# Kernel tuning notes

Hardware: AMD Instinct MI355X
Metric: run time of the kernel (lower is better)

## Reference

```python
import jax, jax.numpy as jnp
import numpy as np

N_USERS = 100000
N_ITEMS = 50000
N = N_USERS + N_ITEMS  # graph nodes
E = 2_400_000
B = 16384
EMB = 64
HID = 128
LN_EPS = 1e-5


def _gcn(x, W, b, src, dst):
    # PyG GCNConv (eval): sym-normalized aggregation with self-loops.
    xw = x @ W                                      # [N, out]
    deg = jnp.ones((N,), x.dtype).at[dst].add(1.0)  # in-degree + self-loop
    dinv = jax.lax.rsqrt(deg)
    norm = dinv[src] * dinv[dst]                    # [E]
    msg = xw[src] * norm[:, None]                   # [E, out] gather
    out = jax.ops.segment_sum(msg, dst, num_segments=N)
    out = out + xw * (dinv * dinv)[:, None]         # self-loop term (norm_ii = 1/deg_i)
    return out + b


def _ln(h, g, b):
    mu = jnp.mean(h, axis=-1, keepdims=True)
    var = jnp.mean(jnp.square(h - mu), axis=-1, keepdims=True)
    return (h - mu) * jax.lax.rsqrt(var + LN_EPS) * g + b


def setup_inputs() -> dict:
    key = jax.random.key(0)
    ks = jax.random.split(key, 20)
    f32 = jnp.float32
    def lin(k, fi, fo):
        return jax.random.normal(k, (fi, fo), f32) * (1.0 / np.sqrt(fi))
    inp = {
        "x": jax.random.normal(ks[0], (N, EMB), f32),
        "src": jax.random.randint(ks[1], (E,), 0, N, jnp.int32),
        "dst": jax.random.randint(ks[2], (E,), 0, N, jnp.int32),
        "user_indices": jax.random.randint(ks[3], (B,), 1, N_USERS + 1, jnp.int32),
        "item_indices": jax.random.randint(ks[4], (B,), 1, N_ITEMS + 1, jnp.int32),
        # GCNConv weights
        "W1": lin(ks[5], EMB, HID), "b1": jnp.zeros((HID,), f32),
        "W2": lin(ks[6], HID, EMB), "b2": jnp.zeros((EMB,), f32),
        # MLP head: Linear(128,128)-LN-ReLU-Linear(128,64)-LN-ReLU-Linear(64,1)
        "fcW1": lin(ks[7], 2 * EMB, HID), "fcb1": jnp.zeros((HID,), f32),
        "g1": jnp.ones((HID,), f32), "be1": jnp.zeros((HID,), f32),
        "fcW2": lin(ks[8], HID, HID // 2), "fcb2": jnp.zeros((HID // 2,), f32),
        "g2": jnp.ones((HID // 2,), f32), "be2": jnp.zeros((HID // 2,), f32),
        "fcW3": lin(ks[9], HID // 2, 1), "fcb3": jnp.zeros((1,), f32),
    }
    return inp


def reference(x, src, dst, user_indices, item_indices,
              W1, b1, W2, b2,
              fcW1, fcb1, g1, be1, fcW2, fcb2, g2, be2, fcW3, fcb3):
    # graph path (edge_index and x provided); dropout inactive in eval mode
    h = jax.nn.relu(_gcn(x, W1, b1, src, dst))
    h = _gcn(h, W2, b2, src, dst)                   # [N, EMB]
    user_emb = h[:N_USERS][user_indices - 1]        # [B, EMB]
    item_emb = h[N_USERS:][item_indices - 1]        # [B, EMB]
    c = jnp.concatenate([user_emb, item_emb], axis=1)  # [B, 2*EMB]
    z = jax.nn.relu(_ln(c @ fcW1 + fcb1, g1, be1))
    z = jax.nn.relu(_ln(z @ fcW2 + fcb2, g2, be2))
    z = z @ fcW3 + fcb3                             # [B, 1]
    return jax.nn.sigmoid(z).squeeze()
```

## Files before the change

kernel.cpp:

```cpp
#include <hip/hip_runtime.h>
#include <hip/hip_bf16.h>
#include <math.h>

#define N_USERS_C 100000
#define BK_SHIFT 9
#define BK_NODES 512
#define CPAD 16

typedef __bf16 bf8_t __attribute__((ext_vector_type(8)));
typedef float f32x4 __attribute__((ext_vector_type(4)));

__device__ __forceinline__ unsigned int pack_bf16(float a, float b) {
    __hip_bfloat16 ha = __float2bfloat16(a), hb = __float2bfloat16(b);
    return ((unsigned int)(*(unsigned short*)&hb) << 16) | (unsigned int)(*(unsigned short*)&ha);
}
__device__ __forceinline__ unsigned short bf16_1(float a) {
    __hip_bfloat16 ha = __float2bfloat16(a);
    return *(unsigned short*)&ha;
}
__device__ __forceinline__ float bf_lo(unsigned int u) { return __uint_as_float(u << 16); }
__device__ __forceinline__ float bf_hi(unsigned int u) { return __uint_as_float(u & 0xffff0000u); }

__global__ __launch_bounds__(512) void k_pre(const int* __restrict__ dst, int* __restrict__ chist,
                                             const float* __restrict__ x, unsigned int* __restrict__ xb,
                                             const float* __restrict__ W1, const float* __restrict__ W2,
                                             unsigned int* __restrict__ w1p, unsigned int* __restrict__ w2p,
                                             int E, int nbk, int EB2, int n2, int XB) {
    __shared__ int lcnt[BK_NODES];
    const int bid = blockIdx.x;
    const int t = threadIdx.x;
    if (bid < EB2) {
        if (t < nbk) lcnt[t] = 0;
        __syncthreads();
        int e0 = bid * 4096;
        #pragma unroll
        for (int j = 0; j < 8; ++j) {
            int e = e0 + j * 512 + t;
            if (e < E) atomicAdd(&lcnt[dst[e] >> BK_SHIFT], 1);
        }
        __syncthreads();
        if (t < nbk && lcnt[t]) atomicAdd(&chist[t * CPAD], lcnt[t]);
    } else if (bid < EB2 + XB) {
        int base = (bid - EB2) * 2048;
        #pragma unroll
        for (int j = 0; j < 4; ++j) {
            int i = base + j * 512 + t;
            if (i < n2) {
                float2 v = ((const float2*)x)[i];
                xb[i] = pack_bf16(v.x, v.y);
            }
        }
    } else if (bid == EB2 + XB) {
        #pragma unroll
        for (int j = 0; j < 8; ++j) {
            int i = j * 512 + t;
            int kp = i >> 7, n = i & 127;
            w1p[n * 32 + kp] = pack_bf16(W1[(size_t)(2 * kp) * 128 + n],
                                         W1[(size_t)(2 * kp + 1) * 128 + n]);
        }
    } else {
        #pragma unroll
        for (int j = 0; j < 8; ++j) {
            int i = j * 512 + t;
            int kp = i >> 6, n = i & 63;
            w2p[n * 64 + kp] = pack_bf16(W2[(size_t)(2 * kp) * 64 + n],
                                         W2[(size_t)(2 * kp + 1) * 64 + n]);
        }
    }
}

__global__ __launch_bounds__(512) void k_bin(const int* __restrict__ src,
                                             const int* __restrict__ dst,
                                             const int* __restrict__ chist,
                                             int* __restrict__ bcursor0,
                                             int* __restrict__ pairBuf, int E, int nbk) {
    __shared__ int lcnt[BK_NODES];
    __shared__ int lofs[BK_NODES];
    __shared__ int delta[BK_NODES];
    __shared__ int waveSum[8];
    __shared__ int sPack[4096];
    __shared__ unsigned short sBkt[4096];
    const int t = threadIdx.x;
    const int lane = t & 63;
    const int w = t >> 6;
    const int e0 = blockIdx.x * 4096;
    if (t < nbk) lcnt[t] = 0;
    __syncthreads();

    int mySrc[8], myB[8], myDl[8];
    #pragma unroll
    for (int j = 0; j < 8; ++j) {
        int e = e0 + j * 512 + t;
        if (e < E) {
            int sv = src[e], dv = dst[e];
            mySrc[j] = sv; myB[j] = dv >> BK_SHIFT; myDl[j] = dv & (BK_NODES - 1);
            atomicAdd(&lcnt[myB[j]], 1);
        } else myB[j] = -1;
    }
    __syncthreads();

    int v = (t < nbk) ? lcnt[t] : 0;
    int inc = v;
    #pragma unroll
    for (int off = 1; off < 64; off <<= 1) {
        int n = __shfl_up(inc, off);
        if (lane >= off) inc += n;
    }
    if (lane == 63) waveSum[w] = inc;
    int cv = (t < nbk) ? chist[t * CPAD] : 0;
    int cinc = cv;
    #pragma unroll
    for (int off = 1; off < 64; off <<= 1) {
        int n = __shfl_up(cinc, off);
        if (lane >= off) cinc += n;
    }
    __shared__ int cWaveSum[8];
    if (lane == 63) cWaveSum[w] = cinc;
    __syncthreads();
    int wp = 0, cwp = 0;
    #pragma unroll
    for (int i = 0; i < 8; ++i) {
        wp += (i < w) ? waveSum[i] : 0;
        cwp += (i < w) ? cWaveSum[i] : 0;
    }
    int ex = wp + inc - v;
    int cbase = cwp + cinc - cv;
    if (t < nbk) {
        lofs[t] = ex;
        int gb = cbase + ((v > 0) ? atomicAdd(&bcursor0[t * CPAD], v) : 0);
        delta[t] = gb - ex;
    }
    __syncthreads();

    #pragma unroll
    for (int j = 0; j < 8; ++j) {
        if (myB[j] >= 0) {
            int p = atomicAdd(&lofs[myB[j]], 1);
            sPack[p] = mySrc[j] | (myDl[j] << 18);
            sBkt[p] = (unsigned short)myB[j];
        }
    }
    __syncthreads();
    int total = (E - e0 < 4096) ? (E - e0) : 4096;
    for (int i = t; i < total; i += 512)
        pairBuf[delta[sBkt[i]] + i] = sPack[i];
}

__global__ __launch_bounds__(512) void k_bscatter(const int* __restrict__ pairBuf,
                                                  const int* __restrict__ chist,
                                                  int* __restrict__ rowstart,
                                                  float* __restrict__ dinv,
                                                  int* __restrict__ csr, int N, int E, int nbk) {
    const int b = blockIdx.x;
    const int n0 = b << BK_SHIFT;
    int nn = N - n0; if (nn > BK_NODES) nn = BK_NODES;
    __shared__ int hist[BK_NODES];
    __shared__ int curs[BK_NODES];
    __shared__ int waveSum[8];
    __shared__ int sE0, sE1;
    const int t = threadIdx.x;
    const int lane = t & 63;
    const int w = t >> 6;

    {
        int cv = (t < nbk) ? chist[t * CPAD] : 0;
        int cinc = cv;
        #pragma unroll
        for (int off = 1; off < 64; off <<= 1) {
            int n = __shfl_up(cinc, off);
            if (lane >= off) cinc += n;
        }
        if (lane == 63) waveSum[w] = cinc;
        if (t < nn) hist[t] = 0;
        __syncthreads();
        int cwp = 0;
        #pragma unroll
        for (int i = 0; i < 8; ++i) cwp += (i < w) ? waveSum[i] : 0;
        if (t == b) { sE0 = cwp + cinc - cv; sE1 = cwp + cinc; }
    }
    __syncthreads();
    const int e0 = sE0, e1 = sE1;

    for (int e = e0 + t; e < e1; e += 512)
        atomicAdd(&hist[pairBuf[e] >> 18], 1);
    __syncthreads();

    int v = (t < nn) ? hist[t] : 0;
    int inc = v;
    #pragma unroll
    for (int off = 1; off < 64; off <<= 1) {
        int n = __shfl_up(inc, off);
        if (lane >= off) inc += n;
    }
    if (lane == 63) waveSum[w] = inc;
    __syncthreads();
    int wp = 0;
    #pragma unroll
    for (int i = 0; i < 8; ++i) wp += (i < w) ? waveSum[i] : 0;
    int ex = wp + inc - v;
    if (t < nn) {
        int r = e0 + ex;
        rowstart[n0 + t] = r;
        curs[t] = r;
        dinv[n0 + t] = rsqrtf((float)(v + 1));
    }
    if (b == gridDim.x - 1 && t == 0) rowstart[N] = E;
    __syncthreads();
    for (int e = e0 + t; e < e1; e += 512) {
        int pk = pairBuf[e];
        int pos = atomicAdd(&curs[pk >> 18], 1);
        csr[pos] = pk & 0x3FFFF;
    }
}

__global__ __launch_bounds__(256) void k_gather1(const int* __restrict__ rowstart,
                                                 const int* __restrict__ csr,
                                                 const float* __restrict__ dinv,
                                                 const uint4* __restrict__ xb4,
                                                 unsigned int* __restrict__ outb, int N) {
    const int node = blockIdx.x * 4 + (threadIdx.x >> 6);
    const int l = threadIdx.x & 63;
    if (node >= N) return;
    const int sub = l >> 3;
    const int c = l & 7;
    const int rs = rowstart[node];
    const int re = rowstart[node + 1];

    float acc[8] = {0.f, 0.f, 0.f, 0.f, 0.f, 0.f, 0.f, 0.f};
    for (int base = rs; base < re; base += 64) {
        int idx = base + l;
        int sE = (idx < re) ? csr[idx] : 0;
        float dE = (idx < re) ? dinv[sE] : 0.0f;
        int cnt = re - base; if (cnt > 64) cnt = 64;
        int groups = (cnt + 7) >> 3;
        for (int g = 0; g < groups; ++g) {
            int e = g * 8 + sub;
            int sk = __shfl(sE, e);
            float dk = __shfl(dE, e);
            uint4 u = xb4[(size_t)sk * 8 + c];
            acc[0] += dk * bf_lo(u.x); acc[1] += dk * bf_hi(u.x);
            acc[2] += dk * bf_lo(u.y); acc[3] += dk * bf_hi(u.y);
            acc[4] += dk * bf_lo(u.z); acc[5] += dk * bf_hi(u.z);
            acc[6] += dk * bf_lo(u.w); acc[7] += dk * bf_hi(u.w);
        }
    }
    #pragma unroll
    for (int m = 8; m < 64; m <<= 1)
        #pragma unroll
        for (int i = 0; i < 8; ++i) acc[i] += __shfl_xor(acc[i], m);
    if (sub == 0) {
        float dd = dinv[node];
        float d2 = dd * dd;
        uint4 us = xb4[(size_t)node * 8 + c];
        uint4 o;
        o.x = pack_bf16(dd * acc[0] + d2 * bf_lo(us.x), dd * acc[1] + d2 * bf_hi(us.x));
        o.y = pack_bf16(dd * acc[2] + d2 * bf_lo(us.y), dd * acc[3] + d2 * bf_hi(us.y));
        o.z = pack_bf16(dd * acc[4] + d2 * bf_lo(us.z), dd * acc[5] + d2 * bf_hi(us.z));
        o.w = pack_bf16(dd * acc[6] + d2 * bf_lo(us.w), dd * acc[7] + d2 * bf_hi(us.w));
        ((uint4*)outb)[(size_t)node * 8 + c] = o;
    }
}

__global__ __launch_bounds__(256) void k_layer12(const unsigned int* __restrict__ aggXb,
                                                 const unsigned int* __restrict__ w1p,
                                                 const float* __restrict__ b1,
                                                 const unsigned int* __restrict__ w2p,
                                                 const float* __restrict__ dinv,
                                                 unsigned int* __restrict__ xs2b, int N) {
    __shared__ unsigned int sA[64 * 36];
    __shared__ unsigned int sB[128 * 36];
    __shared__ unsigned int sC[64 * 68];
    const int t = threadIdx.x;
    const int w = t >> 6;
    const int l = t & 63;
    const int n16 = l & 15;
    const int quad = l >> 4;
    const int row0 = blockIdx.x * 64;

    for (int i = t; i < 512; i += 256) {
        int r = i >> 3, c = i & 7;
        int row = row0 + r;
        uint4 u = (row < N) ? ((const uint4*)aggXb)[(size_t)row * 8 + c]
                            : make_uint4(0u, 0u, 0u, 0u);
        *(uint4*)&sA[r * 36 + c * 4] = u;
    }
    {
        const uint4* w1p4 = (const uint4*)w1p;
        for (int j = t; j < 1024; j += 256) {
            int n = j >> 3, kp4 = j & 7;
            *(uint4*)&sB[n * 36 + kp4 * 4] = w1p4[j];
        }
    }
    __syncthreads();

    f32x4 acc[8];
    #pragma unroll
    for (int nt = 0; nt < 8; ++nt) acc[nt] = (f32x4){0.f, 0.f, 0.f, 0.f};
    {
        const int am = w * 16 + n16;
        bf8_t a0 = *(const bf8_t*)&sA[am * 36 + quad * 4];
        bf8_t a1 = *(const bf8_t*)&sA[am * 36 + 16 + quad * 4];
        #pragma unroll
        for (int nt = 0; nt < 8; ++nt) {
            bf8_t b0 = *(const bf8_t*)&sB[(nt * 16 + n16) * 36 + quad * 4];
            bf8_t b1v = *(const bf8_t*)&sB[(nt * 16 + n16) * 36 + 16 + quad * 4];
            acc[nt] = __builtin_amdgcn_mfma_f32_16x16x32_bf16(a0, b0, acc[nt], 0, 0, 0);
            acc[nt] = __builtin_amdgcn_mfma_f32_16x16x32_bf16(a1, b1v, acc[nt], 0, 0, 0);
        }
    }
    __syncthreads();

    {
        unsigned short* sC16 = (unsigned short*)sC;
        #pragma unroll
        for (int nt = 0; nt < 8; ++nt) {
            int col = nt * 16 + n16;
            float bv = b1[col];
            #pragma unroll
            for (int reg = 0; reg < 4; ++reg) {
                int r = w * 16 + quad * 4 + reg;
                sC16[r * 136 + col] = bf16_1(fmaxf(acc[nt][reg] + bv, 0.f));
            }
        }
    }
    {
        const uint4* w2p4 = (const uint4*)w2p;
        for (int j = t; j < 1024; j += 256) {
            int n = j >> 4, kp4 = j & 15;
            *(uint4*)&sB[n * 68 + kp4 * 4] = w2p4[j];
        }
    }
    __syncthreads();

    f32x4 acc2[4];
    #pragma unroll
    for (int nt = 0; nt < 4; ++nt) acc2[nt] = (f32x4){0.f, 0.f, 0.f, 0.f};
    {
        const int am = w * 16 + n16;
        #pragma unroll
        for (int ks = 0; ks < 4; ++ks) {
            bf8_t a = *(const bf8_t*)&sC[am * 68 + ks * 16 + quad * 4];
            #pragma unroll
            for (int nt = 0; nt < 4; ++nt) {
                bf8_t b = *(const bf8_t*)&sB[(nt * 16 + n16) * 68 + ks * 16 + quad * 4];
                acc2[nt] = __builtin_amdgcn_mfma_f32_16x16x32_bf16(a, b, acc2[nt], 0, 0, 0);
            }
        }
    }

    __syncthreads();
    {
        unsigned short* sA16 = (unsigned short*)sA;
        #pragma unroll
        for (int reg = 0; reg < 4; ++reg) {
            int r = w * 16 + quad * 4 + reg;
            int row = row0 + r;
            float dd = (row < N) ? dinv[row] : 0.f;
            #pragma unroll
            for (int nt = 0; nt < 4; ++nt)
                sA16[r * 72 + nt * 16 + n16] = bf16_1(acc2[nt][reg] * dd);
        }
    }
    __syncthreads();
    for (int i = t; i < 512; i += 256) {
        int r = i >> 3, c = i & 7;
        int row = row0 + r;
        if (row < N)
            ((uint4*)xs2b)[(size_t)row * 8 + c] = *(uint4*)&sA[r * 36 + c * 4];
    }
}

__global__ __launch_bounds__(256) void k_gather_pairs(const int* __restrict__ rowstart,
                                                      const int* __restrict__ csr,
                                                      const float* __restrict__ dinv,
                                                      const uint4* __restrict__ xs2b4,
                                                      const float* __restrict__ b2,
                                                      const int* __restrict__ ui,
                                                      const int* __restrict__ ii,
                                                      float* __restrict__ cB, int B) {
    const int wave = threadIdx.x >> 6;
    const int b = blockIdx.x * 2 + (wave >> 1);
    const int half = wave & 1;
    const int l = threadIdx.x & 63;
    const int sub = l >> 3;
    const int c = l & 7;
    if (b >= B) return;
    const int node = (half == 0) ? (ui[b] - 1) : (N_USERS_C + ii[b] - 1);
    const int rs = rowstart[node];
    const int re = rowstart[node + 1];

    float acc[8] = {0.f, 0.f, 0.f, 0.f, 0.f, 0.f, 0.f, 0.f};
    for (int base = rs; base < re; base += 64) {
        int idx = base + l;
        int sE = (idx < re) ? csr[idx] : 0;
        float vE = (idx < re) ? 1.0f : 0.0f;
        int cnt = re - base; if (cnt > 64) cnt = 64;
        int groups = (cnt + 7) >> 3;
        for (int g = 0; g < groups; ++g) {
            int e = g * 8 + sub;
            int sk = __shfl(sE, e);
            float vk = __shfl(vE, e);
            uint4 u = xs2b4[(size_t)sk * 8 + c];
            acc[0] += vk * bf_lo(u.x); acc[1] += vk * bf_hi(u.x);
            acc[2] += vk * bf_lo(u.y); acc[3] += vk * bf_hi(u.y);
            acc[4] += vk * bf_lo(u.z); acc[5] += vk * bf_hi(u.z);
            acc[6] += vk * bf_lo(u.w); acc[7] += vk * bf_hi(u.w);
        }
    }
    #pragma unroll
    for (int m = 8; m < 64; m <<= 1)
        #pragma unroll
        for (int i = 0; i < 8; ++i) acc[i] += __shfl_xor(acc[i], m);
    if (sub == 0) {
        float dd = dinv[node];
        uint4 us = xs2b4[(size_t)node * 8 + c];
        float4 s0, s1;
        s0.x = bf_lo(us.x); s0.y = bf_hi(us.x); s0.z = bf_lo(us.y); s0.w = bf_hi(us.y);
        s1.x = bf_lo(us.z); s1.y = bf_hi(us.z); s1.z = bf_lo(us.w); s1.w = bf_hi(us.w);
        float4 bb0 = ((const float4*)b2)[c * 2];
        float4 bb1 = ((const float4*)b2)[c * 2 + 1];
        float4 o0, o1;
        o0.x = dd * (acc[0] + s0.x) + bb0.x;
        o0.y = dd * (acc[1] + s0.y) + bb0.y;
        o0.z = dd * (acc[2] + s0.z) + bb0.z;
        o0.w = dd * (acc[3] + s0.w) + bb0.w;
        o1.x = dd * (acc[4] + s1.x) + bb1.x;
        o1.y = dd * (acc[5] + s1.y) + bb1.y;
        o1.z = dd * (acc[6] + s1.z) + bb1.z;
        o1.w = dd * (acc[7] + s1.w) + bb1.w;
        ((float4*)cB)[(size_t)b * 32 + half * 16 + c * 2] = o0;
        ((float4*)cB)[(size_t)b * 32 + half * 16 + c * 2 + 1] = o1;
    }
}

__global__ __launch_bounds__(256) void k_mlp(const float* __restrict__ cB,
                                             const float* __restrict__ fcW1, const float* __restrict__ fcb1,
                                             const float* __restrict__ g1,   const float* __restrict__ be1,
                                             const float* __restrict__ fcW2, const float* __restrict__ fcb2,
                                             const float* __restrict__ g2,   const float* __restrict__ be2,
                                             const float* __restrict__ fcW3, const float* __restrict__ fcb3,
                                             float* __restrict__ out) {
    __shared__ float sIn[32 * 128];
    __shared__ float sW[64 * 128];
    const int t = threadIdx.x;
    const int row0 = blockIdx.x * 32;
    const int rg = t >> 4;
    const int cg = t & 15;

    for (int i = t; i < 1024; i += 256) {
        int r = i >> 5, c4 = i & 31;
        *(float4*)&sIn[r * 128 + c4 * 4] = *(const float4*)&cB[(size_t)(row0 + r) * 128 + c4 * 4];
    }

    float acc1[2][8];
    {
        float4 b01 = *(const float4*)&fcb1[cg * 8];
        float4 b23 = *(const float4*)&fcb1[cg * 8 + 4];
        #pragma unroll
        for (int jj = 0; jj < 2; ++jj) {
            acc1[jj][0] = b01.x; acc1[jj][1] = b01.y; acc1[jj][2] = b01.z; acc1[jj][3] = b01.w;
            acc1[jj][4] = b23.x; acc1[jj][5] = b23.y; acc1[jj][6] = b23.z; acc1[jj][7] = b23.w;
        }
    }
    for (int s = 0; s < 2; ++s) {
        __syncthreads();
        for (int i = t; i < 2048; i += 256) {
            int k = i >> 5, c4 = i & 31;
            *(float4*)&sW[k * 128 + c4 * 4] = *(const float4*)&fcW1[(size_t)(64 * s + k) * 128 + c4 * 4];
        }
        __syncthreads();
        for (int k0 = 0; k0 < 64; k0 += 4) {
            float4 a[2];
            #pragma unroll
            for (int jj = 0; jj < 2; ++jj)
                a[jj] = *(const float4*)&sIn[(rg * 2 + jj) * 128 + 64 * s + k0];
            #pragma unroll
            for (int kk = 0; kk < 4; ++kk) {
                float4 w0 = *(const float4*)&sW[(k0 + kk) * 128 + cg * 8];
                float4 w1 = *(const float4*)&sW[(k0 + kk) * 128 + cg * 8 + 4];
                #pragma unroll
                for (int jj = 0; jj < 2; ++jj) {
                    float f = ((const float*)&a[jj])[kk];
                    acc1[jj][0] += f * w0.x; acc1[jj][1] += f * w0.y;
                    acc1[jj][2] += f * w0.z; acc1[jj][3] += f * w0.w;
                    acc1[jj][4] += f * w1.x; acc1[jj][5] += f * w1.y;
                    acc1[jj][6] += f * w1.z; acc1[jj][7] += f * w1.w;
                }
            }
        }
    }
    __syncthreads();

    {
        float4 g01 = *(const float4*)&g1[cg * 8];
        float4 g23 = *(const float4*)&g1[cg * 8 + 4];
        float4 e01 = *(const float4*)&be1[cg * 8];
        float4 e23 = *(const float4*)&be1[cg * 8 + 4];
        float gv[8] = {g01.x, g01.y, g01.z, g01.w, g23.x, g23.y, g23.z, g23.w};
        float ev[8] = {e01.x, e01.y, e01.z, e01.w, e23.x, e23.y, e23.z, e23.w};
        #pragma unroll
        for (int jj = 0; jj < 2; ++jj) {
            float s_ = 0.f, ss = 0.f;
            #pragma unroll
            for (int c = 0; c < 8; ++c) { float v = acc1[jj][c]; s_ += v; ss += v * v; }
            #pragma unroll
            for (int m = 1; m < 16; m <<= 1) { s_ += __shfl_xor(s_, m); ss += __shfl_xor(ss, m); }
            float mu = s_ * (1.0f / 128.0f);
            float var = ss * (1.0f / 128.0f) - mu * mu;
            float rs = rsqrtf(var + 1e-5f);
            #pragma unroll
            for (int c = 0; c < 8; ++c) {
                float z = (acc1[jj][c] - mu) * rs * gv[c] + ev[c];
                sIn[(rg * 2 + jj) * 128 + cg * 8 + c] = fmaxf(z, 0.f);
            }
        }
    }
    __syncthreads();

    for (int i = t; i < 2048; i += 256) {
        int k = i >> 4, c4 = i & 15;
        *(float4*)&sW[k * 64 + c4 * 4] = *(const float4*)&fcW2[(size_t)k * 64 + c4 * 4];
    }
    float acc2[2][4];
    {
        float4 bv = *(const float4*)&fcb2[cg * 4];
        #pragma unroll
        for (int jj = 0; jj < 2; ++jj) {
            acc2[jj][0] = bv.x; acc2[jj][1] = bv.y; acc2[jj][2] = bv.z; acc2[jj][3] = bv.w;
        }
    }
    __syncthreads();
    for (int k0 = 0; k0 < 128; k0 += 4) {
        float4 a[2], w[4];
        #pragma unroll
        for (int jj = 0; jj < 2; ++jj) a[jj] = *(const float4*)&sIn[(rg * 2 + jj) * 128 + k0];
        #pragma unroll
        for (int kk = 0; kk < 4; ++kk) w[kk] = *(const float4*)&sW[(k0 + kk) * 64 + cg * 4];
        #pragma unroll
        for (int jj = 0; jj < 2; ++jj) {
            const float* aj = (const float*)&a[jj];
            #pragma unroll
            for (int kk = 0; kk < 4; ++kk) {
                float f = aj[kk];
                acc2[jj][0] += f * w[kk].x; acc2[jj][1] += f * w[kk].y;
                acc2[jj][2] += f * w[kk].z; acc2[jj][3] += f * w[kk].w;
            }
        }
    }

    {
        float4 gv4 = *(const float4*)&g2[cg * 4];
        float4 ev4 = *(const float4*)&be2[cg * 4];
        float4 w34 = *(const float4*)&fcW3[cg * 4];
        float gv[4] = {gv4.x, gv4.y, gv4.z, gv4.w};
        float ev[4] = {ev4.x, ev4.y, ev4.z, ev4.w};
        float wv[4] = {w34.x, w34.y, w34.z, w34.w};
        float b3 = fcb3[0];
        #pragma unroll
        for (int jj = 0; jj < 2; ++jj) {
            float s_ = 0.f, ss = 0.f;
            #pragma unroll
            for (int c = 0; c < 4; ++c) { float v = acc2[jj][c]; s_ += v; ss += v * v; }
            #pragma unroll
            for (int m = 1; m < 16; m <<= 1) { s_ += __shfl_xor(s_, m); ss += __shfl_xor(ss, m); }
            float mu = s_ * (1.0f / 64.0f);
            float var = ss * (1.0f / 64.0f) - mu * mu;
            float rs = rsqrtf(var + 1e-5f);
            float p = 0.f;
            #pragma unroll
            for (int c = 0; c < 4; ++c) {
                float z = fmaxf((acc2[jj][c] - mu) * rs * gv[c] + ev[c], 0.f);
                p += z * wv[c];
            }
            #pragma unroll
            for (int m = 1; m < 16; m <<= 1) p += __shfl_xor(p, m);
            if (cg == 0) out[row0 + rg * 2 + jj] = 1.0f / (1.0f + expf(-(p + b3)));
        }
    }
}

extern "C" void kernel_launch(void* const* d_in, const int* in_sizes, int n_in,
                              void* d_out, int out_size, void* d_ws, size_t ws_size,
                              hipStream_t stream) {
    const float* x    = (const float*)d_in[0];
    const int*   src  = (const int*)d_in[1];
    const int*   dst  = (const int*)d_in[2];
    const int*   ui   = (const int*)d_in[3];
    const int*   ii   = (const int*)d_in[4];
    const float* W1   = (const float*)d_in[5];
    const float* b1   = (const float*)d_in[6];
    const float* W2   = (const float*)d_in[7];
    const float* b2   = (const float*)d_in[8];
    const float* fcW1 = (const float*)d_in[9];
    const float* fcb1 = (const float*)d_in[10];
    const float* g1   = (const float*)d_in[11];
    const float* be1  = (const float*)d_in[12];
    const float* fcW2 = (const float*)d_in[13];
    const float* fcb2 = (const float*)d_in[14];
    const float* g2   = (const float*)d_in[15];
    const float* be2  = (const float*)d_in[16];
    const float* fcW3 = (const float*)d_in[17];
    const float* fcb3 = (const float*)d_in[18];
    float* out = (float*)d_out;

    const int N = in_sizes[0] / 64;
    const int E = in_sizes[1];
    const int B = in_sizes[3];
    const int NBK = (N + BK_NODES - 1) >> BK_SHIFT;
    const int EB2 = (E + 4095) / 4096;
    const int n2 = N * 32;
    const int XB = (n2 + 2047) / 2048;

    float* ws   = (float*)d_ws;
    float* dinv = ws;
    int* rowstart = (int*)(dinv + N);
    int* csr      = rowstart + (N + 1);
    unsigned int* xb = (unsigned int*)(csr + E);
    unsigned int* bufU = xb + (size_t)N * 32;
    unsigned int* xs2b = bufU + (size_t)N * 32;
    float* cB = (float*)(xs2b + (size_t)N * 32);
    unsigned int* w1p = (unsigned int*)(cB + (size_t)B * 128);
    unsigned int* w2p = w1p + 4096;
    int* pairBuf = (int*)bufU;
    int* chist   = pairBuf + E;
    int* bcursor = chist + 512 * CPAD;
    unsigned int* aggXb = bufU;

    hipMemsetAsync(chist, 0, 2 * 512 * CPAD * sizeof(int), stream);
    k_pre<<<EB2 + XB + 2, 512, 0, stream>>>(dst, chist, x, xb, W1, W2, w1p, w2p,
                                            E, NBK, EB2, n2, XB);
    k_bin<<<EB2, 512, 0, stream>>>(src, dst, chist, bcursor, pairBuf, E, NBK);
    k_bscatter<<<NBK, 512, 0, stream>>>(pairBuf, chist, rowstart, dinv, csr, N, E, NBK);

    k_gather1<<<(N + 3) / 4, 256, 0, stream>>>(rowstart, csr, dinv, (const uint4*)xb, aggXb, N);

    k_layer12<<<(N + 63) / 64, 256, 0, stream>>>(aggXb, w1p, b1, w2p, dinv, xs2b, N);

    k_gather_pairs<<<(B + 1) / 2, 256, 0, stream>>>(rowstart, csr, dinv, (const uint4*)xs2b,
                                                    b2, ui, ii, cB, B);

    k_mlp<<<B / 32, 256, 0, stream>>>(cB, fcW1, fcb1, g1, be1,
                                      fcW2, fcb2, g2, be2, fcW3, fcb3, out);
}
```

Before: 336.2 us.

## Prescale node features by dinv in bscatter and software-pipeline gather loads

The bf16 node features are pre-multiplied by their own deg^-1/2 inside k_bscatter, so k_gather1 no longer does a per-edge dinv gather or multiply, and the self-loop term becomes dd*(acc+self). Both gather kernels now prefetch the next edge group's feature row before accumulating the current one, and they load the self row and dinv early to overlap latency. The cost is an extra read-modify-write pass over xb in bscatter and an additional bf16 rounding of the scaled features.

```diff
diff --git a/kernel.cpp b/kernel.cpp
--- a/kernel.cpp
+++ b/kernel.cpp
@@ -150,12 +150,15 @@
                                                   const int* __restrict__ chist,
                                                   int* __restrict__ rowstart,
                                                   float* __restrict__ dinv,
-                                                  int* __restrict__ csr, int N, int E, int nbk) {
+                                                  int* __restrict__ csr,
+                                                  unsigned int* __restrict__ xb,
+                                                  int N, int E, int nbk) {
     const int b = blockIdx.x;
     const int n0 = b << BK_SHIFT;
     int nn = N - n0; if (nn > BK_NODES) nn = BK_NODES;
     __shared__ int hist[BK_NODES];
     __shared__ int curs[BK_NODES];
+    __shared__ float sdv[BK_NODES];
     __shared__ int waveSum[8];
     __shared__ int sE0, sE1;
     const int t = threadIdx.x;
@@ -202,7 +205,9 @@
         int r = e0 + ex;
         rowstart[n0 + t] = r;
         curs[t] = r;
-        dinv[n0 + t] = rsqrtf((float)(v + 1));
+        float dv = rsqrtf((float)(v + 1));
+        dinv[n0 + t] = dv;
+        sdv[t] = dv;
     }
     if (b == gridDim.x - 1 && t == 0) rowstart[N] = E;
     __syncthreads();
@@ -210,6 +215,19 @@
         int pk = pairBuf[e];
         int pos = atomicAdd(&curs[pk >> 18], 1);
         csr[pos] = pk & 0x3FFFF;
+    }
+    {
+        uint4* xb4 = (uint4*)(xb + (size_t)n0 * 32);
+        int tot = nn * 8;
+        for (int j = t; j < tot; j += 512) {
+            float dv = sdv[j >> 3];
+            uint4 u = xb4[j];
+            u.x = pack_bf16(dv * bf_lo(u.x), dv * bf_hi(u.x));
+            u.y = pack_bf16(dv * bf_lo(u.y), dv * bf_hi(u.y));
+            u.z = pack_bf16(dv * bf_lo(u.z), dv * bf_hi(u.z));
+            u.w = pack_bf16(dv * bf_lo(u.w), dv * bf_hi(u.w));
+            xb4[j] = u;
+        }
     }
 }
 
@@ -225,23 +243,29 @@
     const int c = l & 7;
     const int rs = rowstart[node];
     const int re = rowstart[node + 1];
+    uint4 us = xb4[(size_t)node * 8 + c];
+    float dd = dinv[node];
 
     float acc[8] = {0.f, 0.f, 0.f, 0.f, 0.f, 0.f, 0.f, 0.f};
     for (int base = rs; base < re; base += 64) {
         int idx = base + l;
         int sE = (idx < re) ? csr[idx] : 0;
-        float dE = (idx < re) ? dinv[sE] : 0.0f;
         int cnt = re - base; if (cnt > 64) cnt = 64;
         int groups = (cnt + 7) >> 3;
+        int sk = __shfl(sE, sub);
+        uint4 u = xb4[(size_t)sk * 8 + c];
         for (int g = 0; g < groups; ++g) {
-            int e = g * 8 + sub;
-            int sk = __shfl(sE, e);
-            float dk = __shfl(dE, e);
-            uint4 u = xb4[(size_t)sk * 8 + c];
-            acc[0] += dk * bf_lo(u.x); acc[1] += dk * bf_hi(u.x);
-            acc[2] += dk * bf_lo(u.y); acc[3] += dk * bf_hi(u.y);
-            acc[4] += dk * bf_lo(u.z); acc[5] += dk * bf_hi(u.z);
-            acc[6] += dk * bf_lo(u.w); acc[7] += dk * bf_hi(u.w);
+            uint4 ucur = u;
+            if (g + 1 < groups) {
+                int skn = __shfl(sE, (g + 1) * 8 + sub);
+                u = xb4[(size_t)skn * 8 + c];
+            }
+            if (g * 8 + sub < cnt) {
+                acc[0] += bf_lo(ucur.x); acc[1] += bf_hi(ucur.x);
+                acc[2] += bf_lo(ucur.y); acc[3] += bf_hi(ucur.y);
+                acc[4] += bf_lo(ucur.z); acc[5] += bf_hi(ucur.z);
+                acc[6] += bf_lo(ucur.w); acc[7] += bf_hi(ucur.w);
+            }
         }
     }
     #pragma unroll
@@ -249,14 +273,11 @@
         #pragma unroll
         for (int i = 0; i < 8; ++i) acc[i] += __shfl_xor(acc[i], m);
     if (sub == 0) {
-        float dd = dinv[node];
-        float d2 = dd * dd;
-        uint4 us = xb4[(size_t)node * 8 + c];
         uint4 o;
-        o.x = pack_bf16(dd * acc[0] + d2 * bf_lo(us.x), dd * acc[1] + d2 * bf_hi(us.x));
-        o.y = pack_bf16(dd * acc[2] + d2 * bf_lo(us.y), dd * acc[3] + d2 * bf_hi(us.y));
-        o.z = pack_bf16(dd * acc[4] + d2 * bf_lo(us.z), dd * acc[5] + d2 * bf_hi(us.z));
-        o.w = pack_bf16(dd * acc[6] + d2 * bf_lo(us.w), dd * acc[7] + d2 * bf_hi(us.w));
+        o.x = pack_bf16(dd * (acc[0] + bf_lo(us.x)), dd * (acc[1] + bf_hi(us.x)));
+        o.y = pack_bf16(dd * (acc[2] + bf_lo(us.y)), dd * (acc[3] + bf_hi(us.y)));
+        o.z = pack_bf16(dd * (acc[4] + bf_lo(us.z)), dd * (acc[5] + bf_hi(us.z)));
+        o.w = pack_bf16(dd * (acc[6] + bf_lo(us.w)), dd * (acc[7] + bf_hi(us.w)));
         ((uint4*)outb)[(size_t)node * 8 + c] = o;
     }
 }
@@ -388,23 +409,29 @@
     const int node = (half == 0) ? (ui[b] - 1) : (N_USERS_C + ii[b] - 1);
     const int rs = rowstart[node];
     const int re = rowstart[node + 1];
+    uint4 us = xs2b4[(size_t)node * 8 + c];
+    float dd = dinv[node];
 
     float acc[8] = {0.f, 0.f, 0.f, 0.f, 0.f, 0.f, 0.f, 0.f};
     for (int base = rs; base < re; base += 64) {
         int idx = base + l;
         int sE = (idx < re) ? csr[idx] : 0;
-        float vE = (idx < re) ? 1.0f : 0.0f;
         int cnt = re - base; if (cnt > 64) cnt = 64;
         int groups = (cnt + 7) >> 3;
+        int sk = __shfl(sE, sub);
+        uint4 u = xs2b4[(size_t)sk * 8 + c];
         for (int g = 0; g < groups; ++g) {
-            int e = g * 8 + sub;
-            int sk = __shfl(sE, e);
-            float vk = __shfl(vE, e);
-            uint4 u = xs2b4[(size_t)sk * 8 + c];
-            acc[0] += vk * bf_lo(u.x); acc[1] += vk * bf_hi(u.x);
-            acc[2] += vk * bf_lo(u.y); acc[3] += vk * bf_hi(u.y);
-            acc[4] += vk * bf_lo(u.z); acc[5] += vk * bf_hi(u.z);
-            acc[6] += vk * bf_lo(u.w); acc[7] += vk * bf_hi(u.w);
+            uint4 ucur = u;
+            if (g + 1 < groups) {
+                int skn = __shfl(sE, (g + 1) * 8 + sub);
+                u = xs2b4[(size_t)skn * 8 + c];
+            }
+            if (g * 8 + sub < cnt) {
+                acc[0] += bf_lo(ucur.x); acc[1] += bf_hi(ucur.x);
+                acc[2] += bf_lo(ucur.y); acc[3] += bf_hi(ucur.y);
+                acc[4] += bf_lo(ucur.z); acc[5] += bf_hi(ucur.z);
+                acc[6] += bf_lo(ucur.w); acc[7] += bf_hi(ucur.w);
+            }
         }
     }
     #pragma unroll
@@ -412,8 +439,6 @@
         #pragma unroll
         for (int i = 0; i < 8; ++i) acc[i] += __shfl_xor(acc[i], m);
     if (sub == 0) {
-        float dd = dinv[node];
-        uint4 us = xs2b4[(size_t)node * 8 + c];
         float4 s0, s1;
         s0.x = bf_lo(us.x); s0.y = bf_hi(us.x); s0.z = bf_lo(us.y); s0.w = bf_hi(us.y);
         s1.x = bf_lo(us.z); s1.y = bf_hi(us.z); s1.z = bf_lo(us.w); s1.w = bf_hi(us.w);
@@ -630,7 +655,7 @@
     k_pre<<<EB2 + XB + 2, 512, 0, stream>>>(dst, chist, x, xb, W1, W2, w1p, w2p,
                                             E, NBK, EB2, n2, XB);
     k_bin<<<EB2, 512, 0, stream>>>(src, dst, chist, bcursor, pairBuf, E, NBK);
-    k_bscatter<<<NBK, 512, 0, stream>>>(pairBuf, chist, rowstart, dinv, csr, N, E, NBK);
+    k_bscatter<<<NBK, 512, 0, stream>>>(pairBuf, chist, rowstart, dinv, csr, xb, N, E, NBK);
 
     k_gather1<<<(N + 3) / 4, 256, 0, stream>>>(rowstart, csr, dinv, (const uint4*)xb, aggXb, N);
 
```

New measurement: 335.8 us. No clear change (-0.1%).
